# Kernel optimization log

Measured on AMD Instinct MI355X. Metric: run time of the kernel, lower is better.

## Reference

```python
import jax, jax.numpy as jnp
import numpy as np

HEADS = 16
DIM_HEAD = 64
LN_EPS = 1e-5


def rotate_half(t):
    # '... (j d) -> ... j d' with j=2, then cat(-x2, x1)
    d = t.shape[-1] // 2
    t1, t2 = t[..., :d], t[..., d:]
    return jnp.concatenate([-t2, t1], axis=-1)


def apply_rotary_pos_emb(t, pos):
    # t: (BT, h, L, dh); pos: (L, rotate_dim)
    rd = pos.shape[-1]
    pos = pos[None, None]  # (1, 1, L, rd)
    t_rot, t_pass = t[..., :rd], t[..., rd:]
    t_rot = t_rot * jnp.cos(pos) + rotate_half(t_rot) * jnp.sin(pos)
    return jnp.concatenate([t_rot, t_pass], axis=-1)


def setup_inputs() -> dict:
    key = jax.random.key(0)
    ks = jax.random.split(key, 4)
    B, T, L, D = 2, 8, 1024, 1024
    inner = HEADS * DIM_HEAD
    x = jax.random.normal(ks[0], (B, T * L, D), dtype=jnp.float32)
    gamma = jnp.ones((D,), jnp.float32)
    beta = jnp.zeros((D,), jnp.float32)
    W_qkv = jax.random.normal(ks[1], (D, 3 * inner), jnp.float32) * (D ** -0.5)
    b_qkv = jnp.zeros((3 * inner,), jnp.float32)
    W_out = jax.random.normal(ks[2], (inner, D), jnp.float32) * (inner ** -0.5)
    # standard GPT-NeoX-style rope angles for the spatial axis, rotate_dim=32
    rot_dim = 32
    inv_freq = 1.0 / (10000.0 ** (jnp.arange(0, rot_dim, 2, dtype=jnp.float32) / rot_dim))
    freqs = jnp.arange(L, dtype=jnp.float32)[:, None] * inv_freq[None, :]  # (L, 16)
    rotary_pos_emb = jnp.concatenate([freqs, freqs], axis=-1)  # (L, 32)
    return {"x": x, "gamma": gamma, "beta": beta, "W_qkv": W_qkv,
            "b_qkv": b_qkv, "W_out": W_out, "rotary_pos_emb": rotary_pos_emb,
            "T": T, "L": L}


def reference(x, gamma, beta, W_qkv, b_qkv, W_out, rotary_pos_emb, T, L):
    B, _, D = x.shape
    h, dh = HEADS, DIM_HEAD
    scale = dh ** -0.5
    # LayerNorm
    mean = jnp.mean(x, axis=-1, keepdims=True)
    var = jnp.mean(jnp.square(x - mean), axis=-1, keepdims=True)
    xn = (x - mean) * jax.lax.rsqrt(var + LN_EPS) * gamma + beta
    # (B, T*L, D) -> (B*T, L, D)
    xr = xn.reshape(B * T, L, D)
    qkv = xr @ W_qkv + b_qkv  # (BT, L, 3*h*dh)
    q, k, v = jnp.split(qkv, 3, axis=-1)
    def to_heads(t):
        return t.reshape(B * T, L, h, dh).transpose(0, 2, 1, 3)  # (BT, h, L, dh)
    q, k, v = map(to_heads, (q, k, v))
    q = apply_rotary_pos_emb(q, rotary_pos_emb)
    k = apply_rotary_pos_emb(k, rotary_pos_emb)
    sim = jnp.einsum('bhid,bhjd->bhij', q, k) * scale
    attn = jax.nn.softmax(sim.astype(jnp.float32), axis=-1).astype(q.dtype)
    out = jnp.einsum('bhij,bhjd->bhid', attn, v)  # (BT, h, L, dh)
    out = out.transpose(0, 2, 1, 3).reshape(B * T, L, h * dh)
    out = out @ W_out  # (BT, L, D)
    return out.reshape(B, T * L, D)
```

## Files before the change

### kernel.cpp

```cpp
#include <hip/hip_runtime.h>
#include <hip/hip_bf16.h>
#include <stdint.h>

typedef short bf16x8 __attribute__((ext_vector_type(8)));
typedef float f32x4  __attribute__((ext_vector_type(4)));
typedef unsigned short u16x4 __attribute__((ext_vector_type(4)));
typedef unsigned int   u32x2 __attribute__((ext_vector_type(2)));

#define DEV __device__ __forceinline__

DEV ushort f2bf(float f){
  unsigned u = __float_as_uint(f);
  u += 0x7FFFu + ((u >> 16) & 1u);
  return (ushort)(u >> 16);
}
DEV float bf2f(ushort h){ return __uint_as_float(((unsigned)h) << 16); }

DEV unsigned pack_bf16x2(float lo, float hi){
  __hip_bfloat162 r = __float22bfloat162_rn(float2{lo, hi});
  return *(unsigned*)&r;
}

DEV void async16(const void* g, void* l){
  __builtin_amdgcn_global_load_lds((const __attribute__((address_space(1))) void*)g,
                                   (__attribute__((address_space(3))) void*)l, 16, 0, 0);
}

__global__ __launch_bounds__(256) void ln_kernel(const float* __restrict__ x,
    const float* __restrict__ gamma, const float* __restrict__ beta,
    ushort* __restrict__ xn)
{
  int row = blockIdx.x;
  int t = threadIdx.x;
  const float4* xr = (const float4*)(x + (size_t)row * 1024);
  float4 v = xr[t];
  float s  = v.x + v.y + v.z + v.w;
  float s2 = v.x*v.x + v.y*v.y + v.z*v.z + v.w*v.w;
  #pragma unroll
  for (int o = 1; o < 64; o <<= 1) { s += __shfl_xor(s, o); s2 += __shfl_xor(s2, o); }
  __shared__ float red[8];
  int lane = t & 63, wv = t >> 6;
  if (lane == 0) { red[wv] = s; red[4 + wv] = s2; }
  __syncthreads();
  s  = red[0] + red[1] + red[2] + red[3];
  s2 = red[4] + red[5] + red[6] + red[7];
  float mean = s * (1.0f / 1024.0f);
  float var  = s2 * (1.0f / 1024.0f) - mean * mean;
  float rs = rsqrtf(var + 1e-5f);
  const float4* g4 = (const float4*)gamma;
  const float4* b4 = (const float4*)beta;
  float4 g = g4[t], b = b4[t];
  u16x4 o4;
  o4[0] = f2bf((v.x - mean) * rs * g.x + b.x);
  o4[1] = f2bf((v.y - mean) * rs * g.y + b.y);
  o4[2] = f2bf((v.z - mean) * rs * g.z + b.z);
  o4[3] = f2bf((v.w - mean) * rs * g.w + b.w);
  ((u16x4*)(xn + (size_t)row * 1024))[t] = o4;
}

__global__ __launch_bounds__(256) void trans_f32_bf16(const float* __restrict__ A,
    ushort* __restrict__ At, int R, int C)
{
  __shared__ __align__(16) ushort tile[64][65];
  int c0 = blockIdx.x * 64, r0 = blockIdx.y * 64;
  int tx = threadIdx.x & 63, ty = threadIdx.x >> 6;
  #pragma unroll
  for (int i = 0; i < 64; i += 4)
    tile[ty + i][tx] = f2bf(A[(size_t)(r0 + ty + i) * C + c0 + tx]);
  __syncthreads();
  #pragma unroll
  for (int i = 0; i < 64; i += 4)
    At[(size_t)(c0 + ty + i) * R + r0 + tx] = tile[tx][ty + i];
}

__global__ __launch_bounds__(256) void rope_tab(const float* __restrict__ rope,
    float* __restrict__ cs, float* __restrict__ sn)
{
  int i = blockIdx.x * 256 + threadIdx.x;
  int l = i >> 4, d = i & 15;
  float p = rope[l * 32 + d];
  float s, c;
  sincosf(p, &s, &c);
  cs[i] = c; sn[i] = s;
}

template<bool OUT_BF16, bool HAS_BIAS, bool ROPE>
__global__ __launch_bounds__(256, 2) void gemm_bt_kernel(
    const ushort* __restrict__ A, const ushort* __restrict__ Bt,
    const float* __restrict__ bias, void* __restrict__ Cout,
    const float* __restrict__ costab, const float* __restrict__ sntab,
    int M, int N, int K)
{
  __shared__ __align__(16) ushort As[2][128 * 64];
  __shared__ __align__(16) ushort Bs[2][128 * 64];
  const int tid = threadIdx.x, lane = tid & 63, w = tid >> 6;
  const int fr = lane & 15, fg = lane >> 4;
  const int wr = w >> 1, wc = w & 1;
  const int aRow0 = blockIdx.y * 128, bCol0 = blockIdx.x * 128;
  const int srow = lane >> 3;
  const int scol = (((lane & 7) ^ srow) << 4);
  const int swz = (fr & 7) << 4;
  const size_t ldb = (size_t)K * 2;

  f32x4 acc[4][4];
  f32x4 z = {0.f, 0.f, 0.f, 0.f};
  #pragma unroll
  for (int mf = 0; mf < 4; ++mf)
    #pragma unroll
    for (int nf = 0; nf < 4; ++nf) acc[mf][nf] = z;

  auto stage = [&](int buf, int k0) {
    const char* ab = (const char*)A + (size_t)aRow0 * ldb + (size_t)k0 * 2;
    const char* bb = (const char*)Bt + (size_t)bCol0 * ldb + (size_t)k0 * 2;
    #pragma unroll
    for (int i = 0; i < 8; ++i) {
      int idx = w * 8 + i;
      if (idx < 16) {
        async16(ab + (size_t)(idx * 8 + srow) * ldb + scol, (char*)As[buf] + idx * 1024);
      } else {
        int c = idx - 16;
        async16(bb + (size_t)(c * 8 + srow) * ldb + scol, (char*)Bs[buf] + c * 1024);
      }
    }
  };

  stage(0, 0);
  __syncthreads();
  const int nk = K >> 6;
  for (int kt = 0; kt < nk; ++kt) {
    int buf = kt & 1;
    if (kt + 1 < nk) stage(buf ^ 1, (kt + 1) << 6);
    const char* as = (const char*)As[buf];
    const char* bs = (const char*)Bs[buf];
    #pragma unroll
    for (int kc = 0; kc < 2; ++kc) {
      int kb = (kc * 64 + fg * 16) ^ swz;
      bf16x8 a[4], b[4];
      #pragma unroll
      for (int mf = 0; mf < 4; ++mf)
        a[mf] = *(const bf16x8*)(as + (wr * 64 + mf * 16 + fr) * 128 + kb);
      #pragma unroll
      for (int nf = 0; nf < 4; ++nf)
        b[nf] = *(const bf16x8*)(bs + (wc * 64 + nf * 16 + fr) * 128 + kb);
      #pragma unroll
      for (int mf = 0; mf < 4; ++mf)
        #pragma unroll
        for (int nf = 0; nf < 4; ++nf)
          acc[mf][nf] = __builtin_amdgcn_mfma_f32_16x16x32_bf16(a[mf], b[nf], acc[mf][nf], 0, 0, 0);
    }
    __syncthreads();
  }
  #pragma unroll
  for (int pr = 0; pr < 2; ++pr) {
    int nf0 = pr * 2, nf1 = nf0 + 1;
    int gc0 = bCol0 + wc * 64 + nf0 * 16 + fr;
    int gc1 = gc0 + 16;
    float bv0 = HAS_BIAS ? bias[gc0] : 0.0f;
    float bv1 = HAS_BIAS ? bias[gc1] : 0.0f;
    bool rot = ROPE && (pr == 0) && (gc0 < 2048);
    float qs = (ROPE && gc0 < 1024) ? 0.125f : 1.0f;
    #pragma unroll
    for (int mf = 0; mf < 4; ++mf) {
      int gr0 = aRow0 + wr * 64 + mf * 16 + fg * 4;
      #pragma unroll
      for (int r = 0; r < 4; ++r) {
        int gr = gr0 + r;
        float a = acc[mf][nf0][r] + bv0;
        float b = acc[mf][nf1][r] + bv1;
        if (rot) {
          int l = gr & 1023;
          float cs = costab[l * 16 + fr];
          float sn = sntab[l * 16 + fr];
          float an = fmaf(a, cs, -b * sn);
          b = fmaf(b, cs, a * sn);
          a = an;
        }
        a *= qs; b *= qs;
        if (OUT_BF16) {
          ((ushort*)Cout)[(size_t)gr * N + gc0] = f2bf(a);
          ((ushort*)Cout)[(size_t)gr * N + gc1] = f2bf(b);
        } else {
          ((float*)Cout)[(size_t)gr * N + gc0] = a;
          ((float*)Cout)[(size_t)gr * N + gc1] = b;
        }
      }
    }
  }
}

__global__ __launch_bounds__(256) void vtrans_kernel(const ushort* __restrict__ qkv,
                                                     ushort* __restrict__ vT)
{
  __shared__ __align__(16) ushort tile[64][65];
  int bh = blockIdx.x & 255, lt = blockIdx.x >> 8;
  int bt = bh >> 4, h = bh & 15;
  int tx = threadIdx.x & 63, ty = threadIdx.x >> 6;
  const ushort* src = qkv + (size_t)(bt * 1024 + lt * 64) * 3072 + 2048 + h * 64;
  #pragma unroll
  for (int i = 0; i < 64; i += 4)
    tile[ty + i][tx] = src[(size_t)(ty + i) * 3072 + tx];
  __syncthreads();
  ushort* dst = vT + (size_t)bh * 64 * 1024 + lt * 64;
  #pragma unroll
  for (int i = 0; i < 64; i += 4)
    dst[(size_t)(ty + i) * 1024 + tx] = tile[tx][ty + i];
}

__global__ __launch_bounds__(256, 2) void attn_kernel(
    const ushort* __restrict__ qkv, const ushort* __restrict__ vT,
    ushort* __restrict__ aout)
{
  __shared__ __align__(16) ushort Ks[2][64 * 64];
  __shared__ __align__(16) ushort Vs[2][64 * 64];
  __shared__ __align__(16) ushort Ps[4][32 * 64];
  const int tid = threadIdx.x, lane = tid & 63, w = tid >> 6;
  const int fr = lane & 15, fg = lane >> 4;
  const int bh = blockIdx.x & 255, qt = blockIdx.x >> 8;
  const int bt = bh >> 4, h = bh & 15;
  const size_t ld = 3072;
  const ushort* qbase = qkv + (size_t)bt * 1024 * ld + h * 64;
  const ushort* kbase = qbase + 1024;
  const ushort* vtb = vT + (size_t)bh * 64 * 1024;
  const int srow = lane >> 3;
  const int scol = (((lane & 7) ^ srow) << 4);
  const int swz = (fr & 7) << 4;

  bf16x8 qfr[2][2];
  #pragma unroll
  for (int qf = 0; qf < 2; ++qf)
    #pragma unroll
    for (int kc = 0; kc < 2; ++kc) {
      int qrow = qt * 128 + w * 32 + qf * 16 + fr;
      qfr[qf][kc] = *(const bf16x8*)((const char*)(qbase + (size_t)qrow * ld) + kc * 64 + fg * 16);
    }

  f32x4 o[2][4];
  f32x4 z = {0.f, 0.f, 0.f, 0.f};
  #pragma unroll
  for (int a = 0; a < 2; ++a)
    #pragma unroll
    for (int b = 0; b < 4; ++b) o[a][b] = z;
  float m_[2] = {-1e30f, -1e30f}, l_[2] = {0.f, 0.f};

  auto stage = [&](int buf, int t) {
    #pragma unroll
    for (int i = 0; i < 2; ++i) {
      int ch = w * 2 + i;
      async16((const char*)(kbase + (size_t)(t * 64 + ch * 8 + srow) * ld) + scol,
              (char*)Ks[buf] + ch * 1024);
      async16((const char*)(vtb + (size_t)(ch * 8 + srow) * 1024) + t * 128 + scol,
              (char*)Vs[buf] + ch * 1024);
    }
  };

  stage(0, 0);
  __syncthreads();
  for (int t = 0; t < 16; ++t) {
    int cur = t & 1;
    if (t + 1 < 16) stage(cur ^ 1, t + 1);

    bf16x8 kf[4][2];
    #pragma unroll
    for (int kvf = 0; kvf < 4; ++kvf)
      #pragma unroll
      for (int kc = 0; kc < 2; ++kc)
        kf[kvf][kc] = *(const bf16x8*)((const char*)Ks[cur] + (kvf * 16 + fr) * 128 +
                                       ((kc * 64 + fg * 16) ^ swz));
    float alpha[2];
    #pragma unroll
    for (int qf = 0; qf < 2; ++qf) {
      f32x4 st[4];
      #pragma unroll
      for (int kvf = 0; kvf < 4; ++kvf) st[kvf] = z;
      __builtin_amdgcn_s_setprio(1);
      #pragma unroll
      for (int kc = 0; kc < 2; ++kc)
        #pragma unroll
        for (int kvf = 0; kvf < 4; ++kvf)
          st[kvf] = __builtin_amdgcn_mfma_f32_16x16x32_bf16(kf[kvf][kc], qfr[qf][kc], st[kvf], 0, 0, 0);
      __builtin_amdgcn_s_setprio(0);
      float mx = -1e30f;
      #pragma unroll
      for (int kvf = 0; kvf < 4; ++kvf)
        #pragma unroll
        for (int r = 0; r < 4; ++r) mx = fmaxf(mx, st[kvf][r]);
      mx = fmaxf(mx, __shfl_xor(mx, 16));
      mx = fmaxf(mx, __shfl_xor(mx, 32));
      float mn = fmaxf(m_[qf], mx);
      alpha[qf] = __expf(m_[qf] - mn);
      m_[qf] = mn;
      float sum = 0.f;
      int qrow = qf * 16 + fr;
      #pragma unroll
      for (int kvf = 0; kvf < 4; ++kvf) {
        float p0 = __expf(st[kvf][0] - mn), p1 = __expf(st[kvf][1] - mn);
        float p2 = __expf(st[kvf][2] - mn), p3 = __expf(st[kvf][3] - mn);
        sum += (p0 + p1) + (p2 + p3);
        u32x2 u;
        u[0] = pack_bf16x2(p0, p1);
        u[1] = pack_bf16x2(p2, p3);
        *(u32x2*)((char*)Ps[w] + qrow * 128 + ((kvf * 32 + fg * 8) ^ swz)) = u;
      }
      sum += __shfl_xor(sum, 16);
      sum += __shfl_xor(sum, 32);
      l_[qf] = l_[qf] * alpha[qf] + sum;
    }
    #pragma unroll
    for (int of = 0; of < 2; ++of) {
      float ar[4];
      #pragma unroll
      for (int r = 0; r < 4; ++r) ar[r] = __shfl(alpha[of], fg * 4 + r);
      #pragma unroll
      for (int cf = 0; cf < 4; ++cf)
        #pragma unroll
        for (int r = 0; r < 4; ++r) o[of][cf][r] *= ar[r];
    }
    __builtin_amdgcn_s_setprio(1);
    #pragma unroll
    for (int kc4 = 0; kc4 < 2; ++kc4) {
      bf16x8 pa[2];
      #pragma unroll
      for (int of = 0; of < 2; ++of)
        pa[of] = *(const bf16x8*)((const char*)Ps[w] + (of * 16 + fr) * 128 +
                                  ((kc4 * 64 + fg * 16) ^ swz));
      #pragma unroll
      for (int cf = 0; cf < 4; ++cf) {
        bf16x8 vb = *(const bf16x8*)((const char*)Vs[cur] + (cf * 16 + fr) * 128 +
                                     ((kc4 * 64 + fg * 16) ^ swz));
        #pragma unroll
        for (int of = 0; of < 2; ++of)
          o[of][cf] = __builtin_amdgcn_mfma_f32_16x16x32_bf16(pa[of], vb, o[of][cf], 0, 0, 0);
      }
    }
    __builtin_amdgcn_s_setprio(0);
    __syncthreads();
  }
  #pragma unroll
  for (int of = 0; of < 2; ++of) {
    float li[4];
    #pragma unroll
    for (int r = 0; r < 4; ++r) li[r] = 1.0f / __shfl(l_[of], fg * 4 + r);
    #pragma unroll
    for (int cf = 0; cf < 4; ++cf)
      #pragma unroll
      for (int r = 0; r < 4; ++r) {
        int grow_ = bt * 1024 + qt * 128 + w * 32 + of * 16 + fg * 4 + r;
        int gcol  = h * 64 + cf * 16 + fr;
        aout[(size_t)grow_ * 1024 + gcol] = f2bf(o[of][cf][r] * li[r]);
      }
  }
}

extern "C" void kernel_launch(void* const* d_in, const int* in_sizes, int n_in,
                              void* d_out, int out_size, void* d_ws, size_t ws_size,
                              hipStream_t stream)
{
  const float* x     = (const float*)d_in[0];
  const float* gamma = (const float*)d_in[1];
  const float* beta  = (const float*)d_in[2];
  const float* Wqkv  = (const float*)d_in[3];
  const float* bqkv  = (const float*)d_in[4];
  const float* Wout  = (const float*)d_in[5];
  const float* rope  = (const float*)d_in[6];

  char* ws = (char*)d_ws;
  ushort* xn   = (ushort*)(ws + 0);
  ushort* qkvb = (ushort*)(ws + 33554432ULL);
  ushort* vT   = (ushort*)(ws + 134217728ULL);
  ushort* Wqt  = (ushort*)(ws + 167772160ULL);
  ushort* Wot  = (ushort*)(ws + 174063616ULL);
  float* costab = (float*)(ws + 176160768ULL);
  float* sntab  = (float*)(ws + 176226304ULL);
  ushort* aout = xn;

  ln_kernel<<<16384, 256, 0, stream>>>(x, gamma, beta, xn);
  trans_f32_bf16<<<dim3(48, 16), 256, 0, stream>>>(Wqkv, Wqt, 1024, 3072);
  trans_f32_bf16<<<dim3(16, 16), 256, 0, stream>>>(Wout, Wot, 1024, 1024);
  rope_tab<<<64, 256, 0, stream>>>(rope, costab, sntab);
  gemm_bt_kernel<true, true, true><<<dim3(24, 128), 256, 0, stream>>>(
      xn, Wqt, bqkv, (void*)qkvb, costab, sntab, 16384, 3072, 1024);
  vtrans_kernel<<<4096, 256, 0, stream>>>(qkvb, vT);
  attn_kernel<<<2048, 256, 0, stream>>>(qkvb, vT, aout);
  gemm_bt_kernel<false, false, false><<<dim3(8, 128), 256, 0, stream>>>(
      aout, Wot, nullptr, d_out, nullptr, nullptr, 16384, 1024, 1024);
}
```

Measured before the change: 365.2 us.

## Use 256x256 GEMM tiles with XCD-aware block remap and exp2 softmax

Replaces the 128x128 GEMM with a 512-thread 256x256-tile kernel. It splits each K-stage into two 32-wide halves with manual vmcnt waits and barriers, so the next loads overlap the MFMAs. Blocks are remapped so neighbouring tiles land on the same XCD for L2 reuse. Separately, the Q scale is folded to 0.125*log2(e) so attention can use the hardware exp2 instead of expf. The larger tile raises register pressure and the manual waitcnt sync is fragile.

```diff
diff --git a/kernel.cpp b/kernel.cpp
--- a/kernel.cpp
+++ b/kernel.cpp
@@ -85,71 +85,97 @@
 }
 
 template<bool OUT_BF16, bool HAS_BIAS, bool ROPE>
-__global__ __launch_bounds__(256, 2) void gemm_bt_kernel(
+__global__ __launch_bounds__(512, 2) void gemm256_kernel(
     const ushort* __restrict__ A, const ushort* __restrict__ Bt,
     const float* __restrict__ bias, void* __restrict__ Cout,
     const float* __restrict__ costab, const float* __restrict__ sntab,
-    int M, int N, int K)
-{
-  __shared__ __align__(16) ushort As[2][128 * 64];
-  __shared__ __align__(16) ushort Bs[2][128 * 64];
+    int M, int N, int K, int nbx)
+{
+  __shared__ __align__(16) ushort As[2][2][256][32];
+  __shared__ __align__(16) ushort Bs[2][2][256][32];
   const int tid = threadIdx.x, lane = tid & 63, w = tid >> 6;
   const int fr = lane & 15, fg = lane >> 4;
-  const int wr = w >> 1, wc = w & 1;
-  const int aRow0 = blockIdx.y * 128, bCol0 = blockIdx.x * 128;
-  const int srow = lane >> 3;
-  const int scol = (((lane & 7) ^ srow) << 4);
-  const int swz = (fr & 7) << 4;
+  const int wr = w >> 2, wc = w & 3;
+
+  int nwg = gridDim.x, cpx = nwg >> 3;
+  int logical = (blockIdx.x & 7) * cpx + (blockIdx.x >> 3);
+  int bx = logical % nbx, by = logical / nbx;
+  const int aRow0 = by * 256, bCol0 = bx * 256;
   const size_t ldb = (size_t)K * 2;
 
-  f32x4 acc[4][4];
+  const int lrow = lane >> 2, lch = lane & 3;
+  const int g0 = w * 2, g1 = w * 2 + 1;
+  const int r0 = g0 * 16 + lrow, r1 = g1 * 16 + lrow;
+  const int sc0 = ((lch ^ ((r0 & 3) ^ ((r0 >> 2) & 3))) << 4);
+  const int sc1 = ((lch ^ ((r1 & 3) ^ ((r1 >> 2) & 3))) << 4);
+  const char* Ab = (const char*)A + (size_t)aRow0 * ldb;
+  const char* Bb = (const char*)Bt + (size_t)bCol0 * ldb;
+  const size_t ga0 = (size_t)r0 * ldb, ga1 = (size_t)r1 * ldb;
+  char* ldsA = (char*)&As[0][0][0][0];
+  char* ldsB = (char*)&Bs[0][0][0][0];
+  const int ld0 = g0 * 1024, ld1 = g1 * 1024;
+
+  int rbA[8], rbB[4];
+  #pragma unroll
+  for (int mf = 0; mf < 8; ++mf) {
+    int rr = wr * 128 + mf * 16 + fr;
+    rbA[mf] = rr * 64 + ((fg ^ ((rr & 3) ^ ((rr >> 2) & 3))) << 4);
+  }
+  #pragma unroll
+  for (int nf = 0; nf < 4; ++nf) {
+    int rr = wc * 64 + nf * 16 + fr;
+    rbB[nf] = rr * 64 + ((fg ^ ((rr & 3) ^ ((rr >> 2) & 3))) << 4);
+  }
+
+  f32x4 acc[8][4];
   f32x4 z = {0.f, 0.f, 0.f, 0.f};
   #pragma unroll
-  for (int mf = 0; mf < 4; ++mf)
+  for (int mf = 0; mf < 8; ++mf)
     #pragma unroll
     for (int nf = 0; nf < 4; ++nf) acc[mf][nf] = z;
 
-  auto stage = [&](int buf, int k0) {
-    const char* ab = (const char*)A + (size_t)aRow0 * ldb + (size_t)k0 * 2;
-    const char* bb = (const char*)Bt + (size_t)bCol0 * ldb + (size_t)k0 * 2;
-    #pragma unroll
-    for (int i = 0; i < 8; ++i) {
-      int idx = w * 8 + i;
-      if (idx < 16) {
-        async16(ab + (size_t)(idx * 8 + srow) * ldb + scol, (char*)As[buf] + idx * 1024);
-      } else {
-        int c = idx - 16;
-        async16(bb + (size_t)(c * 8 + srow) * ldb + scol, (char*)Bs[buf] + c * 1024);
-      }
-    }
+  auto stage = [&](int buf, int kt, int kc) {
+    const char* ak = Ab + (size_t)kt * 128 + kc * 64;
+    const char* bk = Bb + (size_t)kt * 128 + kc * 64;
+    int lo = buf * 32768 + kc * 16384;
+    async16(ak + ga0 + sc0, ldsA + lo + ld0);
+    async16(ak + ga1 + sc1, ldsA + lo + ld1);
+    async16(bk + ga0 + sc0, ldsB + lo + ld0);
+    async16(bk + ga1 + sc1, ldsB + lo + ld1);
   };
 
-  stage(0, 0);
-  __syncthreads();
+  stage(0, 0, 0);
+  stage(0, 0, 1);
+  asm volatile("s_waitcnt vmcnt(4)" ::: "memory");
+  __builtin_amdgcn_s_barrier();
+
   const int nk = K >> 6;
   for (int kt = 0; kt < nk; ++kt) {
     int buf = kt & 1;
-    if (kt + 1 < nk) stage(buf ^ 1, (kt + 1) << 6);
-    const char* as = (const char*)As[buf];
-    const char* bs = (const char*)Bs[buf];
+    bool pre = (kt + 1 < nk);
     #pragma unroll
     for (int kc = 0; kc < 2; ++kc) {
-      int kb = (kc * 64 + fg * 16) ^ swz;
-      bf16x8 a[4], b[4];
-      #pragma unroll
-      for (int mf = 0; mf < 4; ++mf)
-        a[mf] = *(const bf16x8*)(as + (wr * 64 + mf * 16 + fr) * 128 + kb);
-      #pragma unroll
-      for (int nf = 0; nf < 4; ++nf)
-        b[nf] = *(const bf16x8*)(bs + (wc * 64 + nf * 16 + fr) * 128 + kb);
-      #pragma unroll
-      for (int mf = 0; mf < 4; ++mf)
+      const char* ab = ldsA + buf * 32768 + kc * 16384;
+      const char* bb = ldsB + buf * 32768 + kc * 16384;
+      bf16x8 a[8], b[4];
+      #pragma unroll
+      for (int mf = 0; mf < 8; ++mf) a[mf] = *(const bf16x8*)(ab + rbA[mf]);
+      #pragma unroll
+      for (int nf = 0; nf < 4; ++nf) b[nf] = *(const bf16x8*)(bb + rbB[nf]);
+      if (pre) stage(buf ^ 1, kt + 1, kc);
+      __builtin_amdgcn_s_setprio(1);
+      #pragma unroll
+      for (int mf = 0; mf < 8; ++mf)
         #pragma unroll
         for (int nf = 0; nf < 4; ++nf)
           acc[mf][nf] = __builtin_amdgcn_mfma_f32_16x16x32_bf16(a[mf], b[nf], acc[mf][nf], 0, 0, 0);
-    }
-    __syncthreads();
-  }
+      __builtin_amdgcn_s_setprio(0);
+      if (pre) { asm volatile("s_waitcnt vmcnt(4)" ::: "memory"); }
+      else     { asm volatile("s_waitcnt vmcnt(0)" ::: "memory"); }
+      __builtin_amdgcn_s_barrier();
+    }
+  }
+
   #pragma unroll
   for (int pr = 0; pr < 2; ++pr) {
     int nf0 = pr * 2, nf1 = nf0 + 1;
@@ -158,10 +184,10 @@
     float bv0 = HAS_BIAS ? bias[gc0] : 0.0f;
     float bv1 = HAS_BIAS ? bias[gc1] : 0.0f;
     bool rot = ROPE && (pr == 0) && (gc0 < 2048);
-    float qs = (ROPE && gc0 < 1024) ? 0.125f : 1.0f;
-    #pragma unroll
-    for (int mf = 0; mf < 4; ++mf) {
-      int gr0 = aRow0 + wr * 64 + mf * 16 + fg * 4;
+    float qs = (ROPE && gc0 < 1024) ? 0.18033688f : 1.0f;
+    #pragma unroll
+    for (int mf = 0; mf < 8; ++mf) {
+      int gr0 = aRow0 + wr * 128 + mf * 16 + fg * 4;
       #pragma unroll
       for (int r = 0; r < 4; ++r) {
         int gr = gr0 + r;
@@ -170,9 +196,9 @@
         if (rot) {
           int l = gr & 1023;
           float cs = costab[l * 16 + fr];
-          float sn = sntab[l * 16 + fr];
-          float an = fmaf(a, cs, -b * sn);
-          b = fmaf(b, cs, a * sn);
+          float snv = sntab[l * 16 + fr];
+          float an = fmaf(a, cs, -b * snv);
+          b = fmaf(b, cs, a * snv);
           a = an;
         }
         a *= qs; b *= qs;
@@ -287,14 +313,16 @@
       mx = fmaxf(mx, __shfl_xor(mx, 16));
       mx = fmaxf(mx, __shfl_xor(mx, 32));
       float mn = fmaxf(m_[qf], mx);
-      alpha[qf] = __expf(m_[qf] - mn);
+      alpha[qf] = __builtin_amdgcn_exp2f(m_[qf] - mn);
       m_[qf] = mn;
       float sum = 0.f;
       int qrow = qf * 16 + fr;
       #pragma unroll
       for (int kvf = 0; kvf < 4; ++kvf) {
-        float p0 = __expf(st[kvf][0] - mn), p1 = __expf(st[kvf][1] - mn);
-        float p2 = __expf(st[kvf][2] - mn), p3 = __expf(st[kvf][3] - mn);
+        float p0 = __builtin_amdgcn_exp2f(st[kvf][0] - mn);
+        float p1 = __builtin_amdgcn_exp2f(st[kvf][1] - mn);
+        float p2 = __builtin_amdgcn_exp2f(st[kvf][2] - mn);
+        float p3 = __builtin_amdgcn_exp2f(st[kvf][3] - mn);
         sum += (p0 + p1) + (p2 + p3);
         u32x2 u;
         u[0] = pack_bf16x2(p0, p1);
@@ -377,10 +405,10 @@
   trans_f32_bf16<<<dim3(48, 16), 256, 0, stream>>>(Wqkv, Wqt, 1024, 3072);
   trans_f32_bf16<<<dim3(16, 16), 256, 0, stream>>>(Wout, Wot, 1024, 1024);
   rope_tab<<<64, 256, 0, stream>>>(rope, costab, sntab);
-  gemm_bt_kernel<true, true, true><<<dim3(24, 128), 256, 0, stream>>>(
-      xn, Wqt, bqkv, (void*)qkvb, costab, sntab, 16384, 3072, 1024);
+  gemm256_kernel<true, true, true><<<768, 512, 0, stream>>>(
+      xn, Wqt, bqkv, (void*)qkvb, costab, sntab, 16384, 3072, 1024, 12);
   vtrans_kernel<<<4096, 256, 0, stream>>>(qkvb, vT);
   attn_kernel<<<2048, 256, 0, stream>>>(qkvb, vT, aout);
-  gemm_bt_kernel<false, false, false><<<dim3(8, 128), 256, 0, stream>>>(
-      aout, Wot, nullptr, d_out, nullptr, nullptr, 16384, 1024, 1024);
-}
+  gemm256_kernel<false, false, false><<<256, 512, 0, stream>>>(
+      aout, Wot, nullptr, d_out, nullptr, nullptr, 16384, 1024, 1024, 4);
+}
```

After: 329.6 us. 9.7% less time.
